# Kernel optimization log

Hardware: AMD Instinct MI355X
Metric: run time of the kernel (lower is better)

Reference implementation:

```python
import jax, jax.numpy as jnp
import numpy as np

D_MODEL = 1024
NUM_HEADS = 16
SCALE = 1.0 / np.sqrt(D_MODEL // NUM_HEADS)  # matches sqrt(d_model // num_heads)


def setup_inputs() -> dict:
    key = jax.random.key(0)
    ks = jax.random.split(key, 7)
    B, S, D = 4, 2048, D_MODEL
    std = 1.0 / np.sqrt(D)
    return {
        "x": jax.random.normal(ks[0], (B, S, D), dtype=jnp.float32),
        "Wq": jax.random.normal(ks[1], (D, D), dtype=jnp.float32) * std,
        "bq": jnp.zeros((D,), dtype=jnp.float32),
        "Wk": jax.random.normal(ks[2], (D, D), dtype=jnp.float32) * std,
        "bk": jnp.zeros((D,), dtype=jnp.float32),
        "Wv": jax.random.normal(ks[3], (D, D), dtype=jnp.float32) * std,
        "bv": jnp.zeros((D,), dtype=jnp.float32),
    }


def reference(x, Wq, bq, Wk, bk, Wv, bv):
    # QKV projections (nn.Linear: x @ W^T + b; here W stored as [in, out] already)
    Q = x @ Wq + bq  # [B, S, D]
    K = x @ Wk + bk
    V = x @ Wv + bv
    scores = jnp.einsum("bsd,btd->bst", Q, K) * SCALE  # [B, S, S]
    S_len = x.shape[1]
    causal = jnp.tril(jnp.ones((S_len, S_len), dtype=bool))
    scores = jnp.where(causal, scores, -jnp.inf)
    attn = jax.nn.softmax(scores, axis=-1)
    return jnp.einsum("bst,btd->bsd", attn, V)
```

## Files before the change

### kernel.cpp

```cpp
#include <hip/hip_runtime.h>
#include <hip/hip_bf16.h>
#include <cstdint>

#define D_MODEL 1024
#define SEQ     2048
#define SCALE   0.125f
#define P_ELEMS 2228224

typedef __attribute__((ext_vector_type(8))) _Float16 f16x8;
typedef __attribute__((ext_vector_type(8))) unsigned short u16x8;
typedef __attribute__((ext_vector_type(4))) unsigned short u16x4;
typedef __attribute__((ext_vector_type(4))) float f32x4;

__device__ __forceinline__ unsigned short f2h(float f) {
  _Float16 h = (_Float16)f;
  return __builtin_bit_cast(unsigned short, h);
}

__device__ __forceinline__ void gll16(const void* g, void* lds_p) {
  __builtin_amdgcn_global_load_lds(
      (const __attribute__((address_space(1))) unsigned int*)(uintptr_t)g,
      (__attribute__((address_space(3))) unsigned int*)(unsigned int)(uintptr_t)lds_p,
      16, 0, 0);
}

#define WAITV8 asm volatile("s_waitcnt vmcnt(8)" ::: "memory")
#define WAITV0 asm volatile("s_waitcnt vmcnt(0)" ::: "memory")
#define WAITL0 asm volatile("s_waitcnt lgkmcnt(0)" ::: "memory")
#define SCHEDB __builtin_amdgcn_sched_barrier(0)
#define BAR    __builtin_amdgcn_s_barrier()

__device__ __forceinline__ void stage_tile(const unsigned short* gA, const unsigned short* gB,
                                           size_t sA, size_t sB,
                                           int k0, unsigned short* buf, int w, int lane) {
  int rl = lane >> 3;
  int sg = ((lane & 7) ^ rl) << 3;
#pragma unroll
  for (int j = 0; j < 4; j++) {
    int c = w * 4 + j;
    int row = c * 8 + rl;
    gll16(gA + (size_t)row * sA + k0 + sg, buf + c * 512);
    gll16(gB + (size_t)row * sB + k0 + sg, buf + 8192 + c * 512);
  }
}

__device__ __forceinline__ void load_frags(const unsigned short* buf, int wr, int wc,
                                           int l15, int l4, f16x8 af[4][2], f16x8 bf[4][2]) {
  const unsigned short* bA = buf;
  const unsigned short* bB = buf + 8192;
#pragma unroll
  for (int m = 0; m < 4; m++) {
    int row = wr * 64 + m * 16 + l15, rs = row & 7;
    af[m][0] = *(const f16x8*)(bA + row * 64 + ((l4 ^ rs) << 3));
    af[m][1] = *(const f16x8*)(bA + row * 64 + (((4 + l4) ^ rs) << 3));
  }
#pragma unroll
  for (int n = 0; n < 4; n++) {
    int row = wc * 64 + n * 16 + l15, rs = row & 7;
    bf[n][0] = *(const f16x8*)(bB + row * 64 + ((l4 ^ rs) << 3));
    bf[n][1] = *(const f16x8*)(bB + row * 64 + (((4 + l4) ^ rs) << 3));
  }
}

__device__ __forceinline__ void mfma_tile(f16x8 af[4][2], f16x8 bf[4][2], f32x4 acc[4][4]) {
#pragma unroll
  for (int m = 0; m < 4; m++)
#pragma unroll
    for (int n = 0; n < 4; n++) {
      acc[m][n] = __builtin_amdgcn_mfma_f32_16x16x32_f16(af[m][0], bf[n][0], acc[m][n], 0, 0, 0);
      acc[m][n] = __builtin_amdgcn_mfma_f32_16x16x32_f16(af[m][1], bf[n][1], acc[m][n], 0, 0, 0);
    }
}

__device__ __forceinline__ void gemm_core(const unsigned short* gA, const unsigned short* gB,
                                          size_t sA, size_t sB,
                                          unsigned short* lds0, unsigned short* lds1, int nt,
                                          int w, int lane, int wr, int wc, int l15, int l4,
                                          f32x4 acc[4][4]) {
  stage_tile(gA, gB, sA, sB, 0, lds0, w, lane);
  stage_tile(gA, gB, sA, sB, 64, lds1, w, lane);
  WAITV8; SCHEDB; BAR;
  f16x8 af[4][2], bf[4][2];
  for (int t = 0; t < nt; t += 2) {
    load_frags(lds0, wr, wc, l15, l4, af, bf);
    WAITL0; SCHEDB; BAR;
    if (t + 2 < nt) stage_tile(gA, gB, sA, sB, (t + 2) * 64, lds0, w, lane);
    __builtin_amdgcn_s_setprio(1);
    mfma_tile(af, bf, acc);
    __builtin_amdgcn_s_setprio(0);
    if (t + 2 < nt) { WAITV8; } else { WAITV0; }
    SCHEDB; BAR;
    load_frags(lds1, wr, wc, l15, l4, af, bf);
    WAITL0; SCHEDB; BAR;
    if (t + 3 < nt) stage_tile(gA, gB, sA, sB, (t + 3) * 64, lds1, w, lane);
    __builtin_amdgcn_s_setprio(1);
    mfma_tile(af, bf, acc);
    __builtin_amdgcn_s_setprio(0);
    if (t + 3 < nt) { WAITV8; } else { WAITV0; }
    SCHEDB; BAR;
  }
}

__global__ __launch_bounds__(256) void cvt_x(const float* __restrict__ x,
                                             unsigned short* __restrict__ o, int n8) {
  int i = blockIdx.x * 256 + threadIdx.x;
  if (i >= n8) return;
  const float4* p = (const float4*)x + (size_t)i * 2;
  float4 a = p[0], b = p[1];
  u16x8 r;
  r[0] = f2h(a.x); r[1] = f2h(a.y); r[2] = f2h(a.z); r[3] = f2h(a.w);
  r[4] = f2h(b.x); r[5] = f2h(b.y); r[6] = f2h(b.z); r[7] = f2h(b.w);
  *((u16x8*)o + i) = r;
}

__global__ __launch_bounds__(256) void cvt_w(const float* __restrict__ W0,
                                             const float* __restrict__ W1,
                                             const float* __restrict__ W2,
                                             unsigned short* __restrict__ out) {
  __shared__ float t[32][33];
  int z = blockIdx.z;
  const float* W = (z == 0) ? W0 : (z == 1 ? W1 : W2);
  unsigned short* o = out + (size_t)z * 1024 * 1024;
  int c0 = blockIdx.x * 32, r0 = blockIdx.y * 32;
  int tx = threadIdx.x, ty = threadIdx.y;
  for (int i = 0; i < 4; i++)
    t[ty + 8 * i][tx] = W[(size_t)(r0 + ty + 8 * i) * 1024 + c0 + tx];
  __syncthreads();
  for (int i = 0; i < 4; i++)
    o[(size_t)(c0 + ty + 8 * i) * 1024 + r0 + tx] = f2h(t[tx][ty + 8 * i]);
}

__global__ __launch_bounds__(256) void qkv_gemm(const unsigned short* __restrict__ xb,
                                                const unsigned short* __restrict__ wt,
                                                const float* __restrict__ b0,
                                                const float* __restrict__ b1,
                                                const float* __restrict__ b2,
                                                unsigned short* __restrict__ Qp,
                                                unsigned short* __restrict__ Kp,
                                                unsigned short* __restrict__ vtp) {
  __shared__ unsigned short lds[2][16384];
  int m0 = blockIdx.x * 128;
  int n0 = blockIdx.y * 128;
  int z = n0 >> 10, nz = n0 & 1023;
  const unsigned short* gA = xb + (size_t)m0 * 1024;
  const unsigned short* gB = wt + (size_t)z * 1048576 + (size_t)nz * 1024;
  const float* bias = (z == 0) ? b0 : (z == 1 ? b1 : b2);
  int tid = threadIdx.x, lane = tid & 63, w = tid >> 6;
  int wr = w >> 1, wc = w & 1, l15 = lane & 15, l4 = lane >> 4;
  f32x4 acc[4][4] = {};
  gemm_core(gA, gB, 1024, 1024, &lds[0][0], &lds[1][0], 16, w, lane, wr, wc, l15, l4, acc);

  if (z < 2) {
    unsigned short* O = (z == 0) ? Qp : Kp;
#pragma unroll
    for (int m = 0; m < 4; m++)
#pragma unroll
      for (int n = 0; n < 4; n++) {
        int cl = wc * 64 + n * 16 + l15;
        float bv = bias[nz + cl];
#pragma unroll
        for (int r = 0; r < 4; r++) {
          int row = m0 + wr * 64 + m * 16 + l4 * 4 + r;
          O[(size_t)row * 1024 + nz + cl] = f2h(acc[m][n][r] + bv);
        }
      }
  } else {
    unsigned short* T = &lds[0][0];
#pragma unroll
    for (int m = 0; m < 4; m++)
#pragma unroll
      for (int n = 0; n < 4; n++) {
        int cl = wc * 64 + n * 16 + l15;
        float bv = bias[nz + cl];
#pragma unroll
        for (int r = 0; r < 4; r++) {
          int rl = wr * 64 + m * 16 + l4 * 4 + r;
          T[cl * 136 + rl] = f2h(acc[m][n][r] + bv);
        }
      }
    __syncthreads();
    int bidx = m0 >> 11, s0 = m0 & 2047;
#pragma unroll
    for (int i = 0; i < 8; i++) {
      int d = w * 32 + i * 4 + (lane >> 4);
      int ch = lane & 15;
      u16x8 v = *(const u16x8*)(T + d * 136 + ch * 8);
      *(u16x8*)(vtp + ((size_t)bidx * 1024 + nz + d) * 2048 + s0 + ch * 8) = v;
    }
  }
}

__global__ __launch_bounds__(256) void qk_scores(const unsigned short* __restrict__ Q,
                                                 const unsigned short* __restrict__ Kb,
                                                 float* __restrict__ sc) {
  __shared__ unsigned short lds[2][16384];
  int b = blockIdx.y;
  int i = blockIdx.x;
  int qt = (int)((sqrtf(8.f * i + 1.f) - 1.f) * 0.5f);
  while ((qt + 1) * (qt + 2) / 2 <= i) qt++;
  while (qt * (qt + 1) / 2 > i) qt--;
  int kt = i - qt * (qt + 1) / 2;
  int Wspan = (qt + 1) << 7;
  const unsigned short* gA = Q  + ((size_t)b * 2048 + qt * 128) * 1024;
  const unsigned short* gB = Kb + ((size_t)b * 2048 + kt * 128) * 1024;
  float* outp = sc + (size_t)b * P_ELEMS + (size_t)16384 * (qt * (qt + 1) / 2);
  int tid = threadIdx.x, lane = tid & 63, w = tid >> 6;
  int wr = w >> 1, wc = w & 1, l15 = lane & 15, l4 = lane >> 4;
  f32x4 acc[4][4] = {};
  gemm_core(gA, gB, 1024, 1024, &lds[0][0], &lds[1][0], 16, w, lane, wr, wc, l15, l4, acc);
#pragma unroll
  for (int m = 0; m < 4; m++)
#pragma unroll
    for (int n = 0; n < 4; n++) {
      int cl = wc * 64 + n * 16 + l15;
      int kv = kt * 128 + cl;
#pragma unroll
      for (int r = 0; r < 4; r++) {
        int rl = wr * 64 + m * 16 + l4 * 4 + r;
        int srow = qt * 128 + rl;
        float v = acc[m][n][r] * SCALE;
        if (kv > srow) v = -1e30f;
        outp[(size_t)rl * Wspan + kv] = v;
      }
    }
}

__global__ __launch_bounds__(256) void softmax_row(const float* __restrict__ sc,
                                                   unsigned short* __restrict__ pb) {
  __shared__ float redm[4];
  __shared__ float reds[4];
  int srow = blockIdx.x;
  int b = srow >> 11, sl = srow & 2047;
  int qt = sl >> 7;
  int Wspan = (qt + 1) << 7;
  size_t rb = (size_t)b * P_ELEMS + (size_t)16384 * (qt * (qt + 1) / 2) + (size_t)(sl & 127) * Wspan;
  const float4* src = (const float4*)(sc + rb);
  int nv = Wspan >> 2;
  int t = threadIdx.x, lane = t & 63, w = t >> 6;
  bool h0 = t < nv, h1 = (t + 256) < nv;
  float4 v0 = make_float4(0, 0, 0, 0), v1 = make_float4(0, 0, 0, 0);
  if (h0) v0 = src[t];
  if (h1) v1 = src[t + 256];
  float mx = -1e30f;
  if (h0) mx = fmaxf(fmaxf(v0.x, v0.y), fmaxf(v0.z, v0.w));
  if (h1) mx = fmaxf(mx, fmaxf(fmaxf(v1.x, v1.y), fmaxf(v1.z, v1.w)));
  for (int off = 1; off < 64; off <<= 1) mx = fmaxf(mx, __shfl_xor(mx, off, 64));
  if (lane == 0) redm[w] = mx;
  __syncthreads();
  mx = fmaxf(fmaxf(redm[0], redm[1]), fmaxf(redm[2], redm[3]));
  float s = 0.f;
  float4 e0, e1;
  if (h0) {
    e0.x = __expf(v0.x - mx); e0.y = __expf(v0.y - mx);
    e0.z = __expf(v0.z - mx); e0.w = __expf(v0.w - mx);
    s += e0.x + e0.y + e0.z + e0.w;
  }
  if (h1) {
    e1.x = __expf(v1.x - mx); e1.y = __expf(v1.y - mx);
    e1.z = __expf(v1.z - mx); e1.w = __expf(v1.w - mx);
    s += e1.x + e1.y + e1.z + e1.w;
  }
  for (int off = 1; off < 64; off <<= 1) s += __shfl_xor(s, off, 64);
  if (lane == 0) reds[w] = s;
  __syncthreads();
  s = reds[0] + reds[1] + reds[2] + reds[3];
  float inv = 1.f / s;
  u16x4* dst = (u16x4*)(pb + rb);
  if (h0) {
    u16x4 o;
    o[0] = f2h(e0.x * inv); o[1] = f2h(e0.y * inv);
    o[2] = f2h(e0.z * inv); o[3] = f2h(e0.w * inv);
    dst[t] = o;
  }
  if (h1) {
    u16x4 o;
    o[0] = f2h(e1.x * inv); o[1] = f2h(e1.y * inv);
    o[2] = f2h(e1.z * inv); o[3] = f2h(e1.w * inv);
    dst[t + 256] = o;
  }
}

__global__ __launch_bounds__(256) void pv_gemm(const unsigned short* __restrict__ pb,
                                               const unsigned short* __restrict__ vtp,
                                               float* __restrict__ outp) {
  __shared__ unsigned short lds[2][16384];
  int p = blockIdx.x;
  int n0 = blockIdx.y * 128;
  int b = blockIdx.z;
  int tid = threadIdx.x, lane = tid & 63, w = tid >> 6;
  int wr = w >> 1, wc = w & 1, l15 = lane & 15, l4 = lane >> 4;
  const unsigned short* gB = vtp + (size_t)b * 1024 * 2048 + (size_t)n0 * 2048;
#pragma unroll
  for (int which = 0; which < 2; which++) {
    int qt = which ? (15 - p) : p;
    int Wspan = (qt + 1) << 7;
    const unsigned short* gA = pb + (size_t)b * P_ELEMS + (size_t)16384 * (qt * (qt + 1) / 2);
    float* O = outp + ((size_t)b * 2048 + qt * 128) * 1024;
    f32x4 acc[4][4] = {};
    gemm_core(gA, gB, Wspan, 2048, &lds[0][0], &lds[1][0], 2 * (qt + 1),
              w, lane, wr, wc, l15, l4, acc);
#pragma unroll
    for (int m = 0; m < 4; m++)
#pragma unroll
      for (int n = 0; n < 4; n++) {
        int cl = n0 + wc * 64 + n * 16 + l15;
#pragma unroll
        for (int r = 0; r < 4; r++) {
          int rl = wr * 64 + m * 16 + l4 * 4 + r;
          O[(size_t)rl * 1024 + cl] = acc[m][n][r];
        }
      }
  }
}

extern "C" void kernel_launch(void* const* d_in, const int* in_sizes, int n_in,
                              void* d_out, int out_size, void* d_ws, size_t ws_size,
                              hipStream_t stream) {
  const float* x  = (const float*)d_in[0];
  const float* Wq = (const float*)d_in[1];
  const float* bq = (const float*)d_in[2];
  const float* Wk = (const float*)d_in[3];
  const float* bk = (const float*)d_in[4];
  const float* Wv = (const float*)d_in[5];
  const float* bv = (const float*)d_in[6];
  float* out = (float*)d_out;

  unsigned short* ws  = (unsigned short*)d_ws;
  unsigned short* wt  = ws;
  unsigned short* Qp  = ws + 3145728;
  unsigned short* Kp  = ws + 11534336;
  unsigned short* vtp = ws + 19922944;
  float* sc           = (float*)(ws + 28311552);
  unsigned short* pb  = ws + 46137344;
  unsigned short* xb  = (unsigned short*)d_out;

  cvt_x<<<4096, 256, 0, stream>>>(x, xb, 1048576);
  cvt_w<<<dim3(32, 32, 3), dim3(32, 8), 0, stream>>>(Wq, Wk, Wv, wt);
  qkv_gemm<<<dim3(64, 24), 256, 0, stream>>>(xb, wt, bq, bk, bv, Qp, Kp, vtp);
  qk_scores<<<dim3(136, 4), 256, 0, stream>>>(Qp, Kp, sc);
  softmax_row<<<8192, 256, 0, stream>>>(sc, pb);
  pv_gemm<<<dim3(8, 8, 4), 256, 0, stream>>>(pb, vtp, out);
}
```

Measured before the change: 156.7 us.

## Enlarge QKV GEMM tiles to 256x256 with 8 waves and fuse conversion kernels

The QKV projection GEMM moves from 128x128 tiles with 4 waves to 256x256 tiles with 8 waves. Each wave now computes a 128x64 sub-tile, reusing B fragments across two A half-loads, and the double-buffered pipeline is reworked to a single-buffer-per-iteration loop. The x and W fp32-to-fp16 conversion kernels are merged into one launch. The V transpose epilogue is split into two halves through LDS. The larger tiles cut global and LDS traffic per FLOP, but they raise register and LDS pressure and leave only 384 blocks to spread across the CUs.

```diff
diff --git a/kernel.cpp b/kernel.cpp
--- a/kernel.cpp
+++ b/kernel.cpp
@@ -30,6 +30,8 @@
 #define SCHEDB __builtin_amdgcn_sched_barrier(0)
 #define BAR    __builtin_amdgcn_s_barrier()
 
+#define MFMA16(a, b, c) __builtin_amdgcn_mfma_f32_16x16x32_f16(a, b, c, 0, 0, 0)
+
 __device__ __forceinline__ void stage_tile(const unsigned short* gA, const unsigned short* gB,
                                            size_t sA, size_t sB,
                                            int k0, unsigned short* buf, int w, int lane) {
@@ -67,8 +69,8 @@
   for (int m = 0; m < 4; m++)
 #pragma unroll
     for (int n = 0; n < 4; n++) {
-      acc[m][n] = __builtin_amdgcn_mfma_f32_16x16x32_f16(af[m][0], bf[n][0], acc[m][n], 0, 0, 0);
-      acc[m][n] = __builtin_amdgcn_mfma_f32_16x16x32_f16(af[m][1], bf[n][1], acc[m][n], 0, 0, 0);
+      acc[m][n] = MFMA16(af[m][0], bf[n][0], acc[m][n]);
+      acc[m][n] = MFMA16(af[m][1], bf[n][1], acc[m][n]);
     }
 }
 
@@ -101,91 +103,169 @@
   }
 }
 
-__global__ __launch_bounds__(256) void cvt_x(const float* __restrict__ x,
-                                             unsigned short* __restrict__ o, int n8) {
-  int i = blockIdx.x * 256 + threadIdx.x;
-  if (i >= n8) return;
-  const float4* p = (const float4*)x + (size_t)i * 2;
-  float4 a = p[0], b = p[1];
-  u16x8 r;
-  r[0] = f2h(a.x); r[1] = f2h(a.y); r[2] = f2h(a.z); r[3] = f2h(a.w);
-  r[4] = f2h(b.x); r[5] = f2h(b.y); r[6] = f2h(b.z); r[7] = f2h(b.w);
-  *((u16x8*)o + i) = r;
-}
-
-__global__ __launch_bounds__(256) void cvt_w(const float* __restrict__ W0,
-                                             const float* __restrict__ W1,
-                                             const float* __restrict__ W2,
-                                             unsigned short* __restrict__ out) {
+__device__ __forceinline__ void stage_tile256(const unsigned short* gA, const unsigned short* gB,
+                                              size_t sA, size_t sB, int k0,
+                                              unsigned short* buf, int w, int lane) {
+  int rl = lane >> 3;
+  int sg = ((lane & 7) ^ rl) << 3;
+#pragma unroll
+  for (int j = 0; j < 4; j++) {
+    int c = w * 4 + j;
+    int row = c * 8 + rl;
+    gll16(gA + (size_t)row * sA + k0 + sg, buf + c * 512);
+    gll16(gB + (size_t)row * sB + k0 + sg, buf + 16384 + c * 512);
+  }
+}
+
+__device__ __forceinline__ void gemm_core256(const unsigned short* gA, const unsigned short* gB,
+                                             size_t sA, size_t sB,
+                                             unsigned short* lds0, unsigned short* lds1, int nt,
+                                             int w, int lane, int wr, int wc, int l15, int l4,
+                                             f32x4 acc[8][4]) {
+  stage_tile256(gA, gB, sA, sB, 0, lds0, w, lane);
+  stage_tile256(gA, gB, sA, sB, 64, lds1, w, lane);
+  WAITV8; SCHEDB; BAR;
+  for (int t = 0; t < nt; t++) {
+    unsigned short* buf = (t & 1) ? lds1 : lds0;
+    const unsigned short* bA = buf;
+    const unsigned short* bB = buf + 16384;
+    f16x8 bf[4][2], af[4][2], ag[4][2];
+#pragma unroll
+    for (int n = 0; n < 4; n++) {
+      int row = wc * 64 + n * 16 + l15, rs = row & 7;
+      bf[n][0] = *(const f16x8*)(bB + row * 64 + ((l4 ^ rs) << 3));
+      bf[n][1] = *(const f16x8*)(bB + row * 64 + (((4 + l4) ^ rs) << 3));
+    }
+#pragma unroll
+    for (int m = 0; m < 4; m++) {
+      int row = wr * 128 + m * 16 + l15, rs = row & 7;
+      af[m][0] = *(const f16x8*)(bA + row * 64 + ((l4 ^ rs) << 3));
+      af[m][1] = *(const f16x8*)(bA + row * 64 + (((4 + l4) ^ rs) << 3));
+    }
+#pragma unroll
+    for (int m = 0; m < 4; m++)
+#pragma unroll
+      for (int n = 0; n < 4; n++) {
+        acc[m][n] = MFMA16(af[m][0], bf[n][0], acc[m][n]);
+        acc[m][n] = MFMA16(af[m][1], bf[n][1], acc[m][n]);
+      }
+#pragma unroll
+    for (int m = 0; m < 4; m++) {
+      int row = wr * 128 + 64 + m * 16 + l15, rs = row & 7;
+      ag[m][0] = *(const f16x8*)(bA + row * 64 + ((l4 ^ rs) << 3));
+      ag[m][1] = *(const f16x8*)(bA + row * 64 + (((4 + l4) ^ rs) << 3));
+    }
+    WAITL0; SCHEDB; BAR;
+    if (t + 2 < nt) stage_tile256(gA, gB, sA, sB, (t + 2) * 64, buf, w, lane);
+    __builtin_amdgcn_s_setprio(1);
+#pragma unroll
+    for (int m = 0; m < 4; m++)
+#pragma unroll
+      for (int n = 0; n < 4; n++) {
+        acc[m + 4][n] = MFMA16(ag[m][0], bf[n][0], acc[m + 4][n]);
+        acc[m + 4][n] = MFMA16(ag[m][1], bf[n][1], acc[m + 4][n]);
+      }
+    __builtin_amdgcn_s_setprio(0);
+    if (t + 2 < nt) { WAITV8; } else { WAITV0; }
+    SCHEDB; BAR;
+  }
+}
+
+__global__ __launch_bounds__(256) void cvt_fused(const float* __restrict__ x,
+                                                 const float* __restrict__ W0,
+                                                 const float* __restrict__ W1,
+                                                 const float* __restrict__ W2,
+                                                 unsigned short* __restrict__ xb,
+                                                 unsigned short* __restrict__ wt) {
   __shared__ float t[32][33];
-  int z = blockIdx.z;
-  const float* W = (z == 0) ? W0 : (z == 1 ? W1 : W2);
-  unsigned short* o = out + (size_t)z * 1024 * 1024;
-  int c0 = blockIdx.x * 32, r0 = blockIdx.y * 32;
-  int tx = threadIdx.x, ty = threadIdx.y;
-  for (int i = 0; i < 4; i++)
-    t[ty + 8 * i][tx] = W[(size_t)(r0 + ty + 8 * i) * 1024 + c0 + tx];
-  __syncthreads();
-  for (int i = 0; i < 4; i++)
-    o[(size_t)(c0 + ty + 8 * i) * 1024 + r0 + tx] = f2h(t[tx][ty + 8 * i]);
-}
-
-__global__ __launch_bounds__(256) void qkv_gemm(const unsigned short* __restrict__ xb,
-                                                const unsigned short* __restrict__ wt,
-                                                const float* __restrict__ b0,
-                                                const float* __restrict__ b1,
-                                                const float* __restrict__ b2,
-                                                unsigned short* __restrict__ Qp,
-                                                unsigned short* __restrict__ Kp,
-                                                unsigned short* __restrict__ vtp) {
-  __shared__ unsigned short lds[2][16384];
-  int m0 = blockIdx.x * 128;
-  int n0 = blockIdx.y * 128;
+  int bid = blockIdx.x;
+  int tid = threadIdx.x;
+  if (bid < 4096) {
+    int i = bid * 256 + tid;
+    const float4* p = (const float4*)x + (size_t)i * 2;
+    float4 a = p[0], b = p[1];
+    u16x8 r;
+    r[0] = f2h(a.x); r[1] = f2h(a.y); r[2] = f2h(a.z); r[3] = f2h(a.w);
+    r[4] = f2h(b.x); r[5] = f2h(b.y); r[6] = f2h(b.z); r[7] = f2h(b.w);
+    *((u16x8*)xb + i) = r;
+  } else {
+    int id = bid - 4096;
+    int z = id >> 10, rem = id & 1023;
+    int bx = rem & 31, by = rem >> 5;
+    const float* W = (z == 0) ? W0 : (z == 1 ? W1 : W2);
+    unsigned short* o = wt + (size_t)z * 1048576;
+    int c0 = bx * 32, r0 = by * 32;
+    int tx = tid & 31, ty = tid >> 5;
+    for (int i = 0; i < 4; i++)
+      t[ty + 8 * i][tx] = W[(size_t)(r0 + ty + 8 * i) * 1024 + c0 + tx];
+    __syncthreads();
+    for (int i = 0; i < 4; i++)
+      o[(size_t)(c0 + ty + 8 * i) * 1024 + r0 + tx] = f2h(t[tx][ty + 8 * i]);
+  }
+}
+
+__global__ __launch_bounds__(512, 2) void qkv_gemm(const unsigned short* __restrict__ xb,
+                                                   const unsigned short* __restrict__ wt,
+                                                   const float* __restrict__ b0,
+                                                   const float* __restrict__ b1,
+                                                   const float* __restrict__ b2,
+                                                   unsigned short* __restrict__ Qp,
+                                                   unsigned short* __restrict__ Kp,
+                                                   unsigned short* __restrict__ vtp) {
+  __shared__ unsigned short lds[2][32768];
+  int m0 = blockIdx.x * 256;
+  int n0 = blockIdx.y * 256;
   int z = n0 >> 10, nz = n0 & 1023;
   const unsigned short* gA = xb + (size_t)m0 * 1024;
   const unsigned short* gB = wt + (size_t)z * 1048576 + (size_t)nz * 1024;
   const float* bias = (z == 0) ? b0 : (z == 1 ? b1 : b2);
   int tid = threadIdx.x, lane = tid & 63, w = tid >> 6;
-  int wr = w >> 1, wc = w & 1, l15 = lane & 15, l4 = lane >> 4;
-  f32x4 acc[4][4] = {};
-  gemm_core(gA, gB, 1024, 1024, &lds[0][0], &lds[1][0], 16, w, lane, wr, wc, l15, l4, acc);
+  int wr = w >> 2, wc = w & 3, l15 = lane & 15, l4 = lane >> 4;
+  f32x4 acc[8][4] = {};
+  gemm_core256(gA, gB, 1024, 1024, &lds[0][0], &lds[1][0], 16, w, lane, wr, wc, l15, l4, acc);
 
   if (z < 2) {
     unsigned short* O = (z == 0) ? Qp : Kp;
 #pragma unroll
-    for (int m = 0; m < 4; m++)
+    for (int m = 0; m < 8; m++)
 #pragma unroll
       for (int n = 0; n < 4; n++) {
         int cl = wc * 64 + n * 16 + l15;
         float bv = bias[nz + cl];
 #pragma unroll
         for (int r = 0; r < 4; r++) {
-          int row = m0 + wr * 64 + m * 16 + l4 * 4 + r;
+          int row = m0 + wr * 128 + m * 16 + l4 * 4 + r;
           O[(size_t)row * 1024 + nz + cl] = f2h(acc[m][n][r] + bv);
         }
       }
   } else {
     unsigned short* T = &lds[0][0];
-#pragma unroll
-    for (int m = 0; m < 4; m++)
-#pragma unroll
-      for (int n = 0; n < 4; n++) {
-        int cl = wc * 64 + n * 16 + l15;
-        float bv = bias[nz + cl];
-#pragma unroll
-        for (int r = 0; r < 4; r++) {
-          int rl = wr * 64 + m * 16 + l4 * 4 + r;
-          T[cl * 136 + rl] = f2h(acc[m][n][r] + bv);
-        }
-      }
-    __syncthreads();
     int bidx = m0 >> 11, s0 = m0 & 2047;
 #pragma unroll
-    for (int i = 0; i < 8; i++) {
-      int d = w * 32 + i * 4 + (lane >> 4);
-      int ch = lane & 15;
-      u16x8 v = *(const u16x8*)(T + d * 136 + ch * 8);
-      *(u16x8*)(vtp + ((size_t)bidx * 1024 + nz + d) * 2048 + s0 + ch * 8) = v;
+    for (int h = 0; h < 2; h++) {
+      __syncthreads();
+      if (wr == h) {
+#pragma unroll
+        for (int m = 0; m < 8; m++)
+#pragma unroll
+          for (int n = 0; n < 4; n++) {
+            int cl = wc * 64 + n * 16 + l15;
+            float bv = bias[nz + cl];
+#pragma unroll
+            for (int r = 0; r < 4; r++) {
+              int rl = m * 16 + l4 * 4 + r;
+              T[cl * 136 + rl] = f2h(acc[m][n][r] + bv);
+            }
+          }
+      }
+      __syncthreads();
+#pragma unroll
+      for (int i = 0; i < 8; i++) {
+        int idx = i * 512 + tid;
+        int d = idx >> 4, ch = idx & 15;
+        u16x8 v = *(const u16x8*)(T + d * 136 + ch * 8);
+        *(u16x8*)(vtp + ((size_t)bidx * 1024 + nz + d) * 2048 + s0 + h * 128 + ch * 8) = v;
+      }
     }
   }
 }
@@ -334,9 +414,8 @@
   unsigned short* pb  = ws + 46137344;
   unsigned short* xb  = (unsigned short*)d_out;
 
-  cvt_x<<<4096, 256, 0, stream>>>(x, xb, 1048576);
-  cvt_w<<<dim3(32, 32, 3), dim3(32, 8), 0, stream>>>(Wq, Wk, Wv, wt);
-  qkv_gemm<<<dim3(64, 24), 256, 0, stream>>>(xb, wt, bq, bk, bv, Qp, Kp, vtp);
+  cvt_fused<<<7168, 256, 0, stream>>>(x, Wq, Wk, Wv, xb, wt);
+  qkv_gemm<<<dim3(32, 12), 512, 0, stream>>>(xb, wt, bq, bk, bv, Qp, Kp, vtp);
   qk_scores<<<dim3(136, 4), 256, 0, stream>>>(Qp, Kp, sc);
   softmax_row<<<8192, 256, 0, stream>>>(sc, pb);
   pv_gemm<<<dim3(8, 8, 4), 256, 0, stream>>>(pb, vtp, out);
```

New measurement: 164.9 us. +5.2%, slower.
